# Optimization experiments

Hardware: AMD Instinct MI355X
Metric: run time of the kernel (lower is better)

The kernel has to match this reference:

```python
import jax, jax.numpy as jnp
import numpy as np

K = 32          # historical_prior_k
EPS_W = 1e-4    # added to squared distance before inverting
EPS_SUM = 1e-9  # clamp on weight normalizer


def setup_inputs() -> dict:
    key = jax.random.key(0)
    k1, k2, k3 = jax.random.split(key, 3)
    points = jax.random.normal(k1, (8, 2048, 64), dtype=jnp.float32)
    features = jax.random.normal(k2, (20000, 64), dtype=jnp.float32)
    targets = jax.random.uniform(k3, (20000,), dtype=jnp.float32)  # in [0,1)
    return {"points": points, "features": features, "targets": targets}


def reference(points, features, targets):
    # points: [B, L, D]; features: [M, D]; targets: [M]
    B, L, D = points.shape
    flat = points.reshape(B * L, D)                      # [N, D]
    # squared Euclidean distances (torch.cdist(...).square())
    qn = jnp.sum(flat * flat, axis=1, keepdims=True)     # [N, 1]
    fn = jnp.sum(features * features, axis=1)            # [M]
    d2 = qn + fn[None, :] - 2.0 * (flat @ features.T)    # [N, M]
    d2 = jnp.maximum(d2, 0.0)
    # k smallest distances -> top_k on negated distances
    neg_d, idx = jax.lax.top_k(-d2, K)                   # [N, K]
    nearest = -neg_d
    w = 1.0 / (nearest + EPS_W)                          # [N, K]
    num = jnp.sum(w * targets[idx], axis=1)              # [N]
    den = jnp.maximum(jnp.sum(w, axis=1), EPS_SUM)
    return (num / den).reshape(B, L)
```

## Files before the change

kernel.cpp:

```cpp
#include <hip/hip_runtime.h>
#include <hip/hip_bf16.h>
#include <math.h>


#define NQ   16384
#define MM   20000
#define DD   64
#define KK   32
#define MPAD 20032
#define NCH  (MPAD / 64)
#define NW   16
#define QB   64
#define CAP  352
#define HS   264

typedef __attribute__((ext_vector_type(8))) short bf16x8;
typedef __attribute__((ext_vector_type(4))) float f32x4;

#define OFF_FH 0
#define SZ_FP  (MPAD * DD * 2)
#define OFF_FL (OFF_FH + SZ_FP)
#define OFF_FN (OFF_FL + SZ_FP)
#define SZ_FN  (MPAD * 4)
#define OFF_QH (OFF_FN + SZ_FN)
#define SZ_QP  (NQ * DD * 2)
#define OFF_QL (OFF_QH + SZ_QP)
#define OFF_QN (OFF_QL + SZ_QP)
#define SZ_QN  (NQ * 4)
#define WS_REQ (OFF_QN + SZ_QN)

__device__ __forceinline__ unsigned int bf16_rne(float x) {
    unsigned int xb = __float_as_uint(x);
    return (xb + 0x7fffu + ((xb >> 16) & 1u)) & 0xffff0000u;
}
__device__ __forceinline__ unsigned enc32(float f) {
    unsigned b = __float_as_uint(f);
    return (b & 0x80000000u) ? ~b : (b | 0x80000000u);
}
__device__ __forceinline__ float dec32(unsigned k) {
    unsigned b = (k & 0x80000000u) ? (k & 0x7FFFFFFFu) : ~k;
    return __uint_as_float(b);
}

__global__ void prep_split(const float* __restrict__ src,
                           unsigned short* __restrict__ ph,
                           unsigned short* __restrict__ pl,
                           float* __restrict__ nrm, int nrows_real) {
    const int e = blockIdx.x * 256 + threadIdx.x;
    const int m = e >> 6;
    const int lane = threadIdx.x & 63;
    const bool real = (m < nrows_real);
    float x = real ? src[e] : 0.f;
    unsigned int hb = bf16_rne(x);
    float xh = __uint_as_float(hb);
    unsigned int lb = bf16_rne(x - xh);
    ph[e] = (unsigned short)(hb >> 16);
    pl[e] = (unsigned short)(lb >> 16);
    float s = x * x;
    #pragma unroll
    for (int o = 32; o >= 1; o >>= 1) s += __shfl_xor(s, o);
    if (lane == 0) nrm[m] = real ? s : __builtin_inff();
}

#define SUBTILE4(c_, t_, EPI_)                                                \
  {                                                                           \
    const int rb_ = (c_) * 64 + (t_) * 16;                                    \
    const unsigned short* phh = Fh + (size_t)(rb_ + q) * DD + kof;            \
    const unsigned short* pll = Fl + (size_t)(rb_ + q) * DD + kof;            \
    const bf16x8 Ah0 = *(const bf16x8*)(phh);                                 \
    const bf16x8 Ah1 = *(const bf16x8*)(phh + 32);                            \
    const bf16x8 Al0 = *(const bf16x8*)(pll);                                 \
    const bf16x8 Al1 = *(const bf16x8*)(pll + 32);                            \
    const f32x4  fnv = *(const f32x4*)(fn + rb_ + hgrp * 4);                  \
    const int rb4 = rb_ + hgrp * 4;                                           \
    _Pragma("unroll")                                                         \
    for (int g = 0; g < 4; ++g) {                                             \
      f32x4 a = {0.f, 0.f, 0.f, 0.f};                                         \
      a = __builtin_amdgcn_mfma_f32_16x16x32_bf16(Ah0, qh0[g], a, 0, 0, 0);   \
      a = __builtin_amdgcn_mfma_f32_16x16x32_bf16(Ah1, qh1[g], a, 0, 0, 0);   \
      a = __builtin_amdgcn_mfma_f32_16x16x32_bf16(Ah0, ql0[g], a, 0, 0, 0);   \
      a = __builtin_amdgcn_mfma_f32_16x16x32_bf16(Ah1, ql1[g], a, 0, 0, 0);   \
      a = __builtin_amdgcn_mfma_f32_16x16x32_bf16(Al0, qh0[g], a, 0, 0, 0);   \
      a = __builtin_amdgcn_mfma_f32_16x16x32_bf16(Al1, qh1[g], a, 0, 0, 0);   \
      a = __builtin_amdgcn_mfma_f32_16x16x32_bf16(Al0, ql0[g], a, 0, 0, 0);   \
      a = __builtin_amdgcn_mfma_f32_16x16x32_bf16(Al1, ql1[g], a, 0, 0, 0);   \
      const float s0 = fnv[0] - 2.f * a[0];                                   \
      const float s1 = fnv[1] - 2.f * a[1];                                   \
      const float s2 = fnv[2] - 2.f * a[2];                                   \
      const float s3 = fnv[3] - 2.f * a[3];                                   \
      EPI_(g, s0, s1, s2, s3, rb4)                                            \
    }                                                                         \
  }

#define EPI_HTOP(g_, s0_, s1_, s2_, s3_, rb4_) {                              \
    (void)(rb4_);                                                             \
    const int r_ = ((g_) * 16 + q) * HS;                                      \
    atomicAdd(&hist[r_ + (enc32(s0_) >> 24)], 1);                             \
    atomicAdd(&hist[r_ + (enc32(s1_) >> 24)], 1);                             \
    atomicAdd(&hist[r_ + (enc32(s2_) >> 24)], 1);                             \
    atomicAdd(&hist[r_ + (enc32(s3_) >> 24)], 1);                             \
}

#define EPI_HMID(g_, s0_, s1_, s2_, s3_, rb4_) {                              \
    (void)(rb4_);                                                             \
    const int r_ = ((g_) * 16 + q) * HS;                                      \
    const unsigned bb_ = (unsigned)bst[g_];                                   \
    const unsigned k0_ = enc32(s0_), k1_ = enc32(s1_);                        \
    const unsigned k2_ = enc32(s2_), k3_ = enc32(s3_);                        \
    if ((k0_ >> 24) == bb_) atomicAdd(&hist[r_ + ((k0_ >> 16) & 0xFFu)], 1);  \
    if ((k1_ >> 24) == bb_) atomicAdd(&hist[r_ + ((k1_ >> 16) & 0xFFu)], 1);  \
    if ((k2_ >> 24) == bb_) atomicAdd(&hist[r_ + ((k2_ >> 16) & 0xFFu)], 1);  \
    if ((k3_ >> 24) == bb_) atomicAdd(&hist[r_ + ((k3_ >> 16) & 0xFFu)], 1);  \
}

#define EPI_GATE(g_, s0_, s1_, s2_, s3_, rb4_) {                              \
    const float tq_ = tauR[g_];                                               \
    const int qq_ = (g_) * 16 + q;                                            \
    const float sv_[4] = {s0_, s1_, s2_, s3_};                                \
    _Pragma("unroll")                                                         \
    for (int j_ = 0; j_ < 4; ++j_) {                                          \
      if (sv_[j_] <= tq_) {                                                   \
        const int p_ = atomicAdd(&cnt[qq_], 1);                               \
        if (p_ < CAP) {                                                       \
          bufd[qq_ * CAP + p_] = sv_[j_];                                     \
          bufi[qq_ * CAP + p_] = (unsigned short)((rb4_) + j_);               \
        }                                                                     \
      }                                                                       \
    }                                                                         \
}

#define SELECT256(qq_, base_, SELB_, BELOW_) {                                 \
    const int b0_ = lane * 4;                                                  \
    const int h0_ = hist[(qq_) * HS + b0_ + 0];                                \
    const int h1_ = hist[(qq_) * HS + b0_ + 1];                                \
    const int h2_ = hist[(qq_) * HS + b0_ + 2];                                \
    const int h3_ = hist[(qq_) * HS + b0_ + 3];                                \
    const int c4_ = h0_ + h1_ + h2_ + h3_;                                     \
    int pref_ = c4_;                                                           \
    _Pragma("unroll")                                                          \
    for (int of_ = 1; of_ < 64; of_ <<= 1) {                                   \
        const int t_ = __shfl_up(pref_, of_);                                  \
        if (lane >= of_) pref_ += t_;                                          \
    }                                                                          \
    const unsigned long long mk_ = __ballot((base_) + pref_ >= KK);            \
    const int sel_ = __builtin_ctzll(mk_ | 0x8000000000000000ull);             \
    const int cb_  = __shfl(pref_ - c4_, sel_) + (base_);                      \
    const int g0_ = __shfl(h0_, sel_), g1_ = __shfl(h1_, sel_);                \
    const int g2_ = __shfl(h2_, sel_);                                         \
    int bs_, bl_;                                                              \
    if      (cb_ + g0_ >= KK)             { bs_ = 0; bl_ = cb_; }              \
    else if (cb_ + g0_ + g1_ >= KK)       { bs_ = 1; bl_ = cb_ + g0_; }        \
    else if (cb_ + g0_ + g1_ + g2_ >= KK) { bs_ = 2; bl_ = cb_ + g0_ + g1_; }  \
    else                                  { bs_ = 3; bl_ = cb_ + g0_ + g1_ + g2_; } \
    SELB_ = sel_ * 4 + bs_;                                                    \
    BELOW_ = bl_;                                                              \
}

__global__ __launch_bounds__(1024) void knn_filter64(
    const unsigned short* __restrict__ Fh, const unsigned short* __restrict__ Fl,
    const float* __restrict__ fn,
    const unsigned short* __restrict__ Qh, const unsigned short* __restrict__ Ql,
    const float* __restrict__ qn,
    const float* __restrict__ targets, float* __restrict__ out)
{
    __shared__ __align__(16) unsigned char pool[QB * CAP * 6];
    __shared__ float tau_f[QB];
    __shared__ int   cnt[QB];
    __shared__ int   bstar[QB];
    __shared__ int   cbel[QB];

    int*            hist = (int*)pool;
    float*          bufd = (float*)pool;
    unsigned short* bufi = (unsigned short*)(pool + QB * CAP * 4);

    const int tid  = threadIdx.x;
    const int lane = tid & 63;
    const int w    = tid >> 6;
    const int qbase = blockIdx.x * QB;
    const int q    = lane & 15;
    const int hgrp = lane >> 4;
    const int kof  = hgrp * 8;

    if (tid < QB) cnt[tid] = 0;
    for (int i = tid; i < QB * HS; i += 1024) hist[i] = 0;

    bf16x8 qh0[4], qh1[4], ql0[4], ql1[4];
    #pragma unroll
    for (int g = 0; g < 4; ++g) {
        const int qrow = qbase + g * 16 + q;
        qh0[g] = *(const bf16x8*)(Qh + (size_t)qrow * DD + kof);
        qh1[g] = *(const bf16x8*)(Qh + (size_t)qrow * DD + kof + 32);
        ql0[g] = *(const bf16x8*)(Ql + (size_t)qrow * DD + kof);
        ql1[g] = *(const bf16x8*)(Ql + (size_t)qrow * DD + kof + 32);
    }
    __syncthreads();

    #pragma unroll
    for (int cc = 0; cc < 4; ++cc) {
        const int chunk = w * 4 + cc;
        #pragma unroll
        for (int t = 0; t < 4; ++t) {
            SUBTILE4(chunk, t, EPI_HTOP)
        }
    }
    __syncthreads();

    #pragma unroll
    for (int e = 0; e < 4; ++e) {
        const int qq = w * 4 + e;
        int sb, bl;
        SELECT256(qq, 0, sb, bl)
        if (lane == 0) { bstar[qq] = sb; cbel[qq] = bl; }
    }
    __syncthreads();

    int bst[4];
    #pragma unroll
    for (int g = 0; g < 4; ++g) bst[g] = bstar[g * 16 + q];

    for (int i = tid; i < QB * HS; i += 1024) hist[i] = 0;
    __syncthreads();

    #pragma unroll
    for (int cc = 0; cc < 4; ++cc) {
        const int chunk = w * 4 + cc;
        #pragma unroll
        for (int t = 0; t < 4; ++t) {
            SUBTILE4(chunk, t, EPI_HMID)
        }
    }
    __syncthreads();

    #pragma unroll
    for (int e = 0; e < 4; ++e) {
        const int qq = w * 4 + e;
        int sb, bl;
        SELECT256(qq, cbel[qq], sb, bl)
        (void)bl;
        if (lane == 0) {
            const unsigned key16 = ((unsigned)bstar[qq] << 8) | (unsigned)sb;
            tau_f[qq] = (key16 >= 0xFFFFu) ? __builtin_inff()
                                           : dec32((key16 + 1u) << 16);
        }
    }
    __syncthreads();

    float tauR[4];
    #pragma unroll
    for (int g = 0; g < 4; ++g) tauR[g] = tau_f[g * 16 + q];

    for (int c = w; c < NCH; c += NW) {
        #pragma unroll
        for (int t = 0; t < 4; ++t) {
            SUBTILE4(c, t, EPI_GATE)
        }
    }
    __syncthreads();

    #pragma unroll
    for (int e = 0; e < 4; ++e) {
        const int q3 = w * 4 + e;
        const int n  = min(cnt[q3], CAP);
        const float qnv = qn[qbase + q3];

        float    ms[6]; unsigned kk[6]; unsigned short miu[6];
        #pragma unroll
        for (int u = 0; u < 6; ++u) {
            const int j = lane + u * 64;
            const bool v = (j < n);
            ms[u]  = v ? bufd[q3 * CAP + j] : __builtin_inff();
            miu[u] = v ? bufi[q3 * CAP + j] : (unsigned short)0xFFFFu;
            kk[u]  = enc32(ms[u]);
        }
        unsigned lo = 0;
        for (int bit = 31; bit >= 0; --bit) {
            const unsigned trial = lo | (1u << bit);
            int c = 0;
            #pragma unroll
            for (int u = 0; u < 6; ++u) c += (kk[u] < trial);
            #pragma unroll
            for (int o = 32; o >= 1; o >>= 1) c += __shfl_xor(c, o);
            if (c < KK) lo = trial;
        }
        int c0 = 0, tcnt = 0;
        #pragma unroll
        for (int u = 0; u < 6; ++u) { c0 += (kk[u] < lo); tcnt += (kk[u] == lo); }
        #pragma unroll
        for (int o = 32; o >= 1; o >>= 1) {
            c0 += __shfl_xor(c0, o); tcnt += __shfl_xor(tcnt, o);
        }
        const int kprime = KK - c0;
        unsigned ilo = 0xFFFFu;
        if (tcnt != kprime) {
            ilo = 0;
            for (int bit = 15; bit >= 0; --bit) {
                const unsigned trial = ilo | (1u << bit);
                int c = 0;
                #pragma unroll
                for (int u = 0; u < 6; ++u)
                    c += ((kk[u] == lo) && ((unsigned)miu[u] < trial));
                #pragma unroll
                for (int o = 32; o >= 1; o >>= 1) c += __shfl_xor(c, o);
                if (c < kprime) ilo = trial;
            }
        }
        float nume = 0.f, deno = 0.f;
        #pragma unroll
        for (int u = 0; u < 6; ++u) {
            const bool inc = (kk[u] < lo) ||
                             ((kk[u] == lo) && ((unsigned)miu[u] <= ilo));
            if (inc) {
                const float d2 = fmaxf(qnv + ms[u], 0.f);
                const float wv = 1.f / (d2 + 1e-4f);
                nume = fmaf(wv, targets[miu[u]], nume);
                deno += wv;
            }
        }
        #pragma unroll
        for (int o = 32; o >= 1; o >>= 1) {
            nume += __shfl_xor(nume, o);
            deno += __shfl_xor(deno, o);
        }
        if (lane == 0) out[qbase + q3] = nume / fmaxf(deno, 1e-9f);
    }
}

#define BQ 32
#define WQ 8
__global__ __launch_bounds__(256) void hp_knn_kernel(
    const float* __restrict__ points, const float* __restrict__ features,
    const float* __restrict__ targets, float* __restrict__ out)
{
    __shared__ __align__(16) float Qs[BQ][DD];
    __shared__ float qn_s[BQ];
    __shared__ float topd[BQ][KK];
    __shared__ int   topi[BQ][KK];
    const int tid = threadIdx.x, lane = tid & 63, wv = tid >> 6, qb = wv * WQ;
    {
        const float4* src = (const float4*)(points + (size_t)blockIdx.x * BQ * DD);
        float4* dst = (float4*)&Qs[0][0];
        #pragma unroll
        for (int i = 0; i < (BQ * DD / 4) / 256; ++i) dst[tid + i * 256] = src[tid + i * 256];
    }
    for (int i = tid; i < BQ * KK; i += 256) { (&topd[0][0])[i] = __builtin_inff(); (&topi[0][0])[i] = 0; }
    __syncthreads();
    if (tid < BQ) {
        float s = 0.f;
        #pragma unroll
        for (int d = 0; d < DD; ++d) s = fmaf(Qs[tid][d], Qs[tid][d], s);
        qn_s[tid] = s;
    }
    __syncthreads();
    for (int c = 0; c < (MM + 63) / 64; ++c) {
        const int m = c * 64 + lane, mc = (m < MM) ? m : (MM - 1);
        float f[DD];
        const float4* fr = (const float4*)(features + (size_t)mc * DD);
        #pragma unroll
        for (int b = 0; b < DD / 4; ++b) { float4 v = fr[b]; f[4*b]=v.x; f[4*b+1]=v.y; f[4*b+2]=v.z; f[4*b+3]=v.w; }
        float fnv = 0.f;
        #pragma unroll
        for (int d = 0; d < DD; ++d) fnv = fmaf(f[d], f[d], fnv);
        float d2v[WQ];
        #pragma unroll
        for (int qi = 0; qi < WQ; ++qi) {
            const float4* qr = (const float4*)&Qs[qb + qi][0];
            float a0=0,a1=0,a2=0,a3=0;
            #pragma unroll
            for (int b = 0; b < DD / 4; ++b) {
                float4 q4 = qr[b];
                a0 = fmaf(q4.x, f[4*b], a0); a1 = fmaf(q4.y, f[4*b+1], a1);
                a2 = fmaf(q4.z, f[4*b+2], a2); a3 = fmaf(q4.w, f[4*b+3], a3);
            }
            float d2 = fmaxf(qn_s[qb+qi] + fnv - 2.f*((a0+a1)+(a2+a3)), 0.f);
            d2v[qi] = (m < MM) ? d2 : __builtin_inff();
        }
        #pragma unroll
        for (int qi = 0; qi < WQ; ++qi) {
            const int q = qb + qi;
            unsigned long long ball = __ballot(d2v[qi] < topd[q][KK-1]);
            while (ball) {
                const int j = __builtin_ctzll(ball); ball &= ball - 1;
                const float dval = __shfl(d2v[qi], j); const int mval = c * 64 + j;
                if (lane < KK) {
                    const float cur = topd[q][lane];
                    if (cur > dval) {
                        const float pd = (lane > 0) ? topd[q][lane-1] : -1.f;
                        const int   pi = (lane > 0) ? topi[q][lane-1] : 0;
                        const bool tp = (pd > dval);
                        topd[q][lane] = tp ? pd : dval; topi[q][lane] = tp ? pi : mval;
                    }
                }
            }
        }
    }
    #pragma unroll
    for (int qi = 0; qi < WQ; ++qi) {
        const int q = qb + qi;
        float wsum = 0.f, wt = 0.f;
        if (lane < KK) {
            const float ww = 1.f / (topd[q][lane] + 1e-4f);
            wsum = ww; wt = ww * targets[topi[q][lane]];
        }
        #pragma unroll
        for (int o = 32; o >= 1; o >>= 1) { wsum += __shfl_xor(wsum, o); wt += __shfl_xor(wt, o); }
        if (lane == 0) out[(size_t)blockIdx.x * BQ + q] = wt / fmaxf(wsum, 1e-9f);
    }
}

extern "C" void kernel_launch(void* const* d_in, const int* in_sizes, int n_in,
                              void* d_out, int out_size, void* d_ws, size_t ws_size,
                              hipStream_t stream) {
    const float* points   = (const float*)d_in[0];
    const float* features = (const float*)d_in[1];
    const float* targets  = (const float*)d_in[2];
    float* out = (float*)d_out;

    if (ws_size < (size_t)WS_REQ) {
        hp_knn_kernel<<<dim3(NQ / BQ), dim3(256), 0, stream>>>(points, features, targets, out);
        return;
    }
    char* ws = (char*)d_ws;
    unsigned short* Fh = (unsigned short*)(ws + OFF_FH);
    unsigned short* Fl = (unsigned short*)(ws + OFF_FL);
    float*          fn = (float*)(ws + OFF_FN);
    unsigned short* Qh = (unsigned short*)(ws + OFF_QH);
    unsigned short* Ql = (unsigned short*)(ws + OFF_QL);
    float*          qnp= (float*)(ws + OFF_QN);

    prep_split<<<dim3(MPAD * DD / 256), dim3(256), 0, stream>>>(features, Fh, Fl, fn, MM);
    prep_split<<<dim3(NQ * DD / 256),  dim3(256), 0, stream>>>(points,   Qh, Ql, qnp, NQ);
    knn_filter64<<<dim3(NQ / QB), dim3(1024), 0, stream>>>(Fh, Fl, fn, Qh, Ql, qnp, targets, out);
}
```

Baseline: 315.8 us.

## Split work so each wave owns one query group and one subtile, syncing periodically

Changes the work split inside the 1024-thread block: each wave now holds registers for a single 16-query group and processes one 16-row feature subtile of every chunk, instead of holding all 64 queries and walking its own chunks. This cuts query register use by a factor of four and keeps all waves streaming the same feature chunks together, with a __syncthreads every two chunks to hold them in lockstep for cache reuse. The cost is fewer MFMAs per feature load, more barriers in the three passes, and more redundant feature loads across waves, though these should mostly hit in L1/L2.

```diff
diff --git a/kernel.cpp b/kernel.cpp
--- a/kernel.cpp
+++ b/kernel.cpp
@@ -13,6 +13,7 @@
 #define QB   64
 #define CAP  352
 #define HS   264
+#define SCH  64
 
 typedef __attribute__((ext_vector_type(8))) short bf16x8;
 typedef __attribute__((ext_vector_type(4))) float f32x4;
@@ -62,9 +63,9 @@
     if (lane == 0) nrm[m] = real ? s : __builtin_inff();
 }
 
-#define SUBTILE4(c_, t_, EPI_)                                                \
+#define SUBTILE1(c_, EPI_)                                                    \
   {                                                                           \
-    const int rb_ = (c_) * 64 + (t_) * 16;                                    \
+    const int rb_ = (c_) * 64 + st * 16;                                      \
     const unsigned short* phh = Fh + (size_t)(rb_ + q) * DD + kof;            \
     const unsigned short* pll = Fl + (size_t)(rb_ + q) * DD + kof;            \
     const bf16x8 Ah0 = *(const bf16x8*)(phh);                                 \
@@ -73,57 +74,50 @@
     const bf16x8 Al1 = *(const bf16x8*)(pll + 32);                            \
     const f32x4  fnv = *(const f32x4*)(fn + rb_ + hgrp * 4);                  \
     const int rb4 = rb_ + hgrp * 4;                                           \
-    _Pragma("unroll")                                                         \
-    for (int g = 0; g < 4; ++g) {                                             \
-      f32x4 a = {0.f, 0.f, 0.f, 0.f};                                         \
-      a = __builtin_amdgcn_mfma_f32_16x16x32_bf16(Ah0, qh0[g], a, 0, 0, 0);   \
-      a = __builtin_amdgcn_mfma_f32_16x16x32_bf16(Ah1, qh1[g], a, 0, 0, 0);   \
-      a = __builtin_amdgcn_mfma_f32_16x16x32_bf16(Ah0, ql0[g], a, 0, 0, 0);   \
-      a = __builtin_amdgcn_mfma_f32_16x16x32_bf16(Ah1, ql1[g], a, 0, 0, 0);   \
-      a = __builtin_amdgcn_mfma_f32_16x16x32_bf16(Al0, qh0[g], a, 0, 0, 0);   \
-      a = __builtin_amdgcn_mfma_f32_16x16x32_bf16(Al1, qh1[g], a, 0, 0, 0);   \
-      a = __builtin_amdgcn_mfma_f32_16x16x32_bf16(Al0, ql0[g], a, 0, 0, 0);   \
-      a = __builtin_amdgcn_mfma_f32_16x16x32_bf16(Al1, ql1[g], a, 0, 0, 0);   \
-      const float s0 = fnv[0] - 2.f * a[0];                                   \
-      const float s1 = fnv[1] - 2.f * a[1];                                   \
-      const float s2 = fnv[2] - 2.f * a[2];                                   \
-      const float s3 = fnv[3] - 2.f * a[3];                                   \
-      EPI_(g, s0, s1, s2, s3, rb4)                                            \
-    }                                                                         \
+    f32x4 a = {0.f, 0.f, 0.f, 0.f};                                           \
+    a = __builtin_amdgcn_mfma_f32_16x16x32_bf16(Ah0, qh0, a, 0, 0, 0);        \
+    a = __builtin_amdgcn_mfma_f32_16x16x32_bf16(Ah1, qh1, a, 0, 0, 0);        \
+    a = __builtin_amdgcn_mfma_f32_16x16x32_bf16(Ah0, ql0, a, 0, 0, 0);        \
+    a = __builtin_amdgcn_mfma_f32_16x16x32_bf16(Ah1, ql1, a, 0, 0, 0);        \
+    a = __builtin_amdgcn_mfma_f32_16x16x32_bf16(Al0, qh0, a, 0, 0, 0);        \
+    a = __builtin_amdgcn_mfma_f32_16x16x32_bf16(Al1, qh1, a, 0, 0, 0);        \
+    a = __builtin_amdgcn_mfma_f32_16x16x32_bf16(Al0, ql0, a, 0, 0, 0);        \
+    a = __builtin_amdgcn_mfma_f32_16x16x32_bf16(Al1, ql1, a, 0, 0, 0);        \
+    const float s0 = fnv[0] - 2.f * a[0];                                     \
+    const float s1 = fnv[1] - 2.f * a[1];                                     \
+    const float s2 = fnv[2] - 2.f * a[2];                                     \
+    const float s3 = fnv[3] - 2.f * a[3];                                     \
+    EPI_(s0, s1, s2, s3, rb4)                                                 \
   }
 
-#define EPI_HTOP(g_, s0_, s1_, s2_, s3_, rb4_) {                              \
+#define EPI_HTOP(s0_, s1_, s2_, s3_, rb4_) {                                  \
     (void)(rb4_);                                                             \
-    const int r_ = ((g_) * 16 + q) * HS;                                      \
-    atomicAdd(&hist[r_ + (enc32(s0_) >> 24)], 1);                             \
-    atomicAdd(&hist[r_ + (enc32(s1_) >> 24)], 1);                             \
-    atomicAdd(&hist[r_ + (enc32(s2_) >> 24)], 1);                             \
-    atomicAdd(&hist[r_ + (enc32(s3_) >> 24)], 1);                             \
-}
-
-#define EPI_HMID(g_, s0_, s1_, s2_, s3_, rb4_) {                              \
+    atomicAdd(&hist[hrow + (enc32(s0_) >> 24)], 1);                           \
+    atomicAdd(&hist[hrow + (enc32(s1_) >> 24)], 1);                           \
+    atomicAdd(&hist[hrow + (enc32(s2_) >> 24)], 1);                           \
+    atomicAdd(&hist[hrow + (enc32(s3_) >> 24)], 1);                           \
+}
+
+#define EPI_HMID(s0_, s1_, s2_, s3_, rb4_) {                                  \
     (void)(rb4_);                                                             \
-    const int r_ = ((g_) * 16 + q) * HS;                                      \
-    const unsigned bb_ = (unsigned)bst[g_];                                   \
+    const unsigned bb_ = (unsigned)bstg;                                      \
     const unsigned k0_ = enc32(s0_), k1_ = enc32(s1_);                        \
     const unsigned k2_ = enc32(s2_), k3_ = enc32(s3_);                        \
-    if ((k0_ >> 24) == bb_) atomicAdd(&hist[r_ + ((k0_ >> 16) & 0xFFu)], 1);  \
-    if ((k1_ >> 24) == bb_) atomicAdd(&hist[r_ + ((k1_ >> 16) & 0xFFu)], 1);  \
-    if ((k2_ >> 24) == bb_) atomicAdd(&hist[r_ + ((k2_ >> 16) & 0xFFu)], 1);  \
-    if ((k3_ >> 24) == bb_) atomicAdd(&hist[r_ + ((k3_ >> 16) & 0xFFu)], 1);  \
-}
-
-#define EPI_GATE(g_, s0_, s1_, s2_, s3_, rb4_) {                              \
-    const float tq_ = tauR[g_];                                               \
-    const int qq_ = (g_) * 16 + q;                                            \
+    if ((k0_ >> 24) == bb_) atomicAdd(&hist[hrow + ((k0_ >> 16) & 0xFFu)], 1);\
+    if ((k1_ >> 24) == bb_) atomicAdd(&hist[hrow + ((k1_ >> 16) & 0xFFu)], 1);\
+    if ((k2_ >> 24) == bb_) atomicAdd(&hist[hrow + ((k2_ >> 16) & 0xFFu)], 1);\
+    if ((k3_ >> 24) == bb_) atomicAdd(&hist[hrow + ((k3_ >> 16) & 0xFFu)], 1);\
+}
+
+#define EPI_GATE(s0_, s1_, s2_, s3_, rb4_) {                                  \
     const float sv_[4] = {s0_, s1_, s2_, s3_};                                \
     _Pragma("unroll")                                                         \
     for (int j_ = 0; j_ < 4; ++j_) {                                          \
-      if (sv_[j_] <= tq_) {                                                   \
-        const int p_ = atomicAdd(&cnt[qq_], 1);                               \
+      if (sv_[j_] <= tauR) {                                                  \
+        const int p_ = atomicAdd(&cnt[qq], 1);                                \
         if (p_ < CAP) {                                                       \
-          bufd[qq_ * CAP + p_] = sv_[j_];                                     \
-          bufi[qq_ * CAP + p_] = (unsigned short)((rb4_) + j_);               \
+          bufd[qq * CAP + p_] = sv_[j_];                                      \
+          bufi[qq * CAP + p_] = (unsigned short)((rb4_) + j_);                \
         }                                                                     \
       }                                                                       \
     }                                                                         \
@@ -156,7 +150,7 @@
     BELOW_ = bl_;                                                              \
 }
 
-__global__ __launch_bounds__(1024) void knn_filter64(
+__global__ __launch_bounds__(1024) void knn_coop64(
     const unsigned short* __restrict__ Fh, const unsigned short* __restrict__ Fl,
     const float* __restrict__ fn,
     const unsigned short* __restrict__ Qh, const unsigned short* __restrict__ Ql,
@@ -176,84 +170,69 @@
     const int tid  = threadIdx.x;
     const int lane = tid & 63;
     const int w    = tid >> 6;
+    const int st   = w >> 2;
+    const int g    = w & 3;
     const int qbase = blockIdx.x * QB;
     const int q    = lane & 15;
     const int hgrp = lane >> 4;
     const int kof  = hgrp * 8;
+    const int qq   = g * 16 + q;
+    const int hrow = qq * HS;
 
     if (tid < QB) cnt[tid] = 0;
     for (int i = tid; i < QB * HS; i += 1024) hist[i] = 0;
 
-    bf16x8 qh0[4], qh1[4], ql0[4], ql1[4];
-    #pragma unroll
-    for (int g = 0; g < 4; ++g) {
-        const int qrow = qbase + g * 16 + q;
-        qh0[g] = *(const bf16x8*)(Qh + (size_t)qrow * DD + kof);
-        qh1[g] = *(const bf16x8*)(Qh + (size_t)qrow * DD + kof + 32);
-        ql0[g] = *(const bf16x8*)(Ql + (size_t)qrow * DD + kof);
-        ql1[g] = *(const bf16x8*)(Ql + (size_t)qrow * DD + kof + 32);
-    }
-    __syncthreads();
-
-    #pragma unroll
-    for (int cc = 0; cc < 4; ++cc) {
-        const int chunk = w * 4 + cc;
-        #pragma unroll
-        for (int t = 0; t < 4; ++t) {
-            SUBTILE4(chunk, t, EPI_HTOP)
-        }
+    const int qrow = qbase + qq;
+    const bf16x8 qh0 = *(const bf16x8*)(Qh + (size_t)qrow * DD + kof);
+    const bf16x8 qh1 = *(const bf16x8*)(Qh + (size_t)qrow * DD + kof + 32);
+    const bf16x8 ql0 = *(const bf16x8*)(Ql + (size_t)qrow * DD + kof);
+    const bf16x8 ql1 = *(const bf16x8*)(Ql + (size_t)qrow * DD + kof + 32);
+    __syncthreads();
+
+    for (int c = 0; c < SCH; ++c) {
+        SUBTILE1(c, EPI_HTOP)
+        if (c & 1) __syncthreads();
     }
     __syncthreads();
 
     #pragma unroll
     for (int e = 0; e < 4; ++e) {
-        const int qq = w * 4 + e;
+        const int qs = w * 4 + e;
         int sb, bl;
-        SELECT256(qq, 0, sb, bl)
-        if (lane == 0) { bstar[qq] = sb; cbel[qq] = bl; }
-    }
-    __syncthreads();
-
-    int bst[4];
-    #pragma unroll
-    for (int g = 0; g < 4; ++g) bst[g] = bstar[g * 16 + q];
+        SELECT256(qs, 0, sb, bl)
+        if (lane == 0) { bstar[qs] = sb; cbel[qs] = bl; }
+    }
+    __syncthreads();
+
+    const int bstg = bstar[qq];
 
     for (int i = tid; i < QB * HS; i += 1024) hist[i] = 0;
     __syncthreads();
 
-    #pragma unroll
-    for (int cc = 0; cc < 4; ++cc) {
-        const int chunk = w * 4 + cc;
-        #pragma unroll
-        for (int t = 0; t < 4; ++t) {
-            SUBTILE4(chunk, t, EPI_HMID)
-        }
+    for (int c = 0; c < SCH; ++c) {
+        SUBTILE1(c, EPI_HMID)
+        if (c & 1) __syncthreads();
     }
     __syncthreads();
 
     #pragma unroll
     for (int e = 0; e < 4; ++e) {
-        const int qq = w * 4 + e;
+        const int qs = w * 4 + e;
         int sb, bl;
-        SELECT256(qq, cbel[qq], sb, bl)
+        SELECT256(qs, cbel[qs], sb, bl)
         (void)bl;
         if (lane == 0) {
-            const unsigned key16 = ((unsigned)bstar[qq] << 8) | (unsigned)sb;
-            tau_f[qq] = (key16 >= 0xFFFFu) ? __builtin_inff()
+            const unsigned key16 = ((unsigned)bstar[qs] << 8) | (unsigned)sb;
+            tau_f[qs] = (key16 >= 0xFFFFu) ? __builtin_inff()
                                            : dec32((key16 + 1u) << 16);
         }
     }
     __syncthreads();
 
-    float tauR[4];
-    #pragma unroll
-    for (int g = 0; g < 4; ++g) tauR[g] = tau_f[g * 16 + q];
-
-    for (int c = w; c < NCH; c += NW) {
-        #pragma unroll
-        for (int t = 0; t < 4; ++t) {
-            SUBTILE4(c, t, EPI_GATE)
-        }
+    const float tauR = tau_f[qq];
+    for (int c = 0; c < NCH; ++c) {
+        SUBTILE1(c, EPI_GATE)
+        if (c & 1) __syncthreads();
     }
     __syncthreads();
 
@@ -429,5 +408,5 @@
 
     prep_split<<<dim3(MPAD * DD / 256), dim3(256), 0, stream>>>(features, Fh, Fl, fn, MM);
     prep_split<<<dim3(NQ * DD / 256),  dim3(256), 0, stream>>>(points,   Qh, Ql, qnp, NQ);
-    knn_filter64<<<dim3(NQ / QB), dim3(1024), 0, stream>>>(Fh, Fl, fn, Qh, Ql, qnp, targets, out);
-}
+    knn_coop64<<<dim3(NQ / QB), dim3(1024), 0, stream>>>(Fh, Fl, fn, Qh, Ql, qnp, targets, out);
+}
```

After: 1.006 ms. 3.18x slower.
